# Optimization experiments

Measured on AMD Instinct MI355X. Metric: run time of the kernel, lower is better.

## Reference

```python
import jax, jax.numpy as jnp
import numpy as np

NCF = 256  # line_emb out features; must equal x channels C


def setup_inputs() -> dict:
    key = jax.random.key(0)
    k1, k2, k3 = jax.random.split(key, 3)
    x = jax.random.normal(k1, (16, 256, 128, 128), dtype=jnp.float32)
    attr = jax.random.normal(k2, (16, 64), dtype=jnp.float32)
    # nn.Linear(1, ncf, bias=False).weight has shape (ncf, 1); flatten to (ncf,)
    w_emb = jax.random.normal(k3, (NCF,), dtype=jnp.float32) / jnp.sqrt(jnp.float32(1.0))
    return {"x": x, "attr": attr, "w_emb": w_emb}


def reference(x, attr, w_emb):
    B, C, H, W = x.shape
    A = attr.reshape(B, -1).shape[1]
    # Linear(1, ncf): attr (B, A, 1) -> (B, A, ncf) is just an outer product
    sa_t = attr.reshape(B, A, 1) * w_emb[None, None, :]          # (B, A, ncf)
    xf = x.reshape(B, C, H * W)                                   # (B, C, HW)
    # tm = semantic_attr_t @ x : contract ncf (== C)
    tm = jnp.einsum('bac,bcn->ban', sa_t, xf)                     # (B, A, HW)
    p = jax.nn.softmax(tm, axis=0)                                # softmax over BATCH dim (dim=0)
    # fattn = semantic_attr (B, ncf, A) @ p (B, A, HW)
    fattn = jnp.einsum('bac,ban->bcn', sa_t, p)                   # (B, C, HW)
    return fattn.reshape(B, C, H, W)
```

## Files before the change

kernel.cpp:

```cpp
#include <hip/hip_runtime.h>
#include <math.h>

#define B_  16
#define C_  256
#define A_  64
#define HW_ 16384
#define HW4 (HW_ / 4)

__global__ __launch_bounds__(256) void k_y(const float* __restrict__ x,
                                           const float* __restrict__ w_emb,
                                           float4* __restrict__ y) {
    __shared__ float w[C_];
    for (int i = threadIdx.x; i < C_; i += 256) w[i] = w_emb[i];
    __syncthreads();

    const int idx = blockIdx.x * 256 + threadIdx.x;
    const int n4  = idx & (HW4 - 1);
    const int b   = idx >> 12;

    const float4* xp = (const float4*)(x + (size_t)b * C_ * HW_) + n4;
    float4 acc = {0.f, 0.f, 0.f, 0.f};
    #pragma unroll 8
    for (int c = 0; c < C_; ++c) {
        const float4 v = xp[(size_t)c * HW4];
        const float wc = w[c];
        acc.x += wc * v.x; acc.y += wc * v.y;
        acc.z += wc * v.z; acc.w += wc * v.w;
    }
    y[idx] = acc;
}

__global__ __launch_bounds__(64) void k_s(const float* __restrict__ y,
                                          const float* __restrict__ attr,
                                          float* __restrict__ s) {
    __shared__ float at[B_ * A_];
    for (int i = threadIdx.x; i < B_ * A_; i += 64) at[i] = attr[i];
    __syncthreads();

    const int n = blockIdx.x * 64 + threadIdx.x;

    float yv[B_];
    #pragma unroll
    for (int b = 0; b < B_; ++b) yv[b] = y[b * HW_ + n];

    float acc[B_];
    #pragma unroll
    for (int b = 0; b < B_; ++b) acc[b] = 0.f;

    for (int a = 0; a < A_; ++a) {
        float t[B_];
        float m = -INFINITY;
        #pragma unroll
        for (int b = 0; b < B_; ++b) {
            t[b] = at[b * A_ + a] * yv[b];
            m = fmaxf(m, t[b]);
        }
        float e[B_];
        float Z = 0.f;
        #pragma unroll
        for (int b = 0; b < B_; ++b) {
            e[b] = expf(t[b] - m);
            Z += e[b];
        }
        const float invZ = 1.f / Z;
        #pragma unroll
        for (int b = 0; b < B_; ++b)
            acc[b] += at[b * A_ + a] * e[b] * invZ;
    }

    #pragma unroll
    for (int b = 0; b < B_; ++b) s[b * HW_ + n] = acc[b];
}

__global__ __launch_bounds__(256) void k_out(const float4* __restrict__ s,
                                             const float* __restrict__ w_emb,
                                             float4* __restrict__ out) {
    __shared__ float w[C_];
    for (int i = threadIdx.x; i < C_; i += 256) w[i] = w_emb[i];
    __syncthreads();

    const int idx = blockIdx.x * 256 + threadIdx.x;
    const int n4  = idx & (HW4 - 1);
    const int b   = idx >> 12;

    const float4 sv = s[idx];
    const size_t base = (size_t)b * C_ * HW4 + n4;
    #pragma unroll 8
    for (int c = 0; c < C_; ++c) {
        const float wc = w[c];
        float4 o;
        o.x = wc * sv.x; o.y = wc * sv.y;
        o.z = wc * sv.z; o.w = wc * sv.w;
        out[base + (size_t)c * HW4] = o;
    }
}

extern "C" void kernel_launch(void* const* d_in, const int* in_sizes, int n_in,
                              void* d_out, int out_size, void* d_ws, size_t ws_size,
                              hipStream_t stream) {
    const float* x     = (const float*)d_in[0];
    const float* attr  = (const float*)d_in[1];
    const float* w_emb = (const float*)d_in[2];
    float* out = (float*)d_out;

    float* y = (float*)d_ws;
    float* s = y + (size_t)B_ * HW_;

    k_y  <<<(B_ * HW4) / 256, 256, 0, stream>>>(x, w_emb, (float4*)y);
    k_s  <<<HW_ / 64,          64, 0, stream>>>(y, attr, s);
    k_out<<<(B_ * HW4) / 256, 256, 0, stream>>>((const float4*)s, w_emb, (float4*)out);
}
```

Before: 523.9 us.

## Split channel reduction and output write across 4 channel quarters for more blocks

The channel contraction in k_y is split into four quarters, each written as a partial sum that k_s adds back together. k_out likewise splits its channel loop into quarters, so both bandwidth-bound kernels launch four times as many blocks to fill more compute units. k_s moves from 64 to 256 threads per block and uses the fast __expf intrinsic. The cost is an extra partial-sum buffer in workspace, extra reads in k_s, and slightly lower accuracy in the exponential.

```diff
diff --git a/kernel.cpp b/kernel.cpp
--- a/kernel.cpp
+++ b/kernel.cpp
@@ -6,42 +6,51 @@
 #define A_  64
 #define HW_ 16384
 #define HW4 (HW_ / 4)
+#define QSPLIT 4
+#define CQ  (C_ / QSPLIT)
 
 __global__ __launch_bounds__(256) void k_y(const float* __restrict__ x,
                                            const float* __restrict__ w_emb,
-                                           float4* __restrict__ y) {
-    __shared__ float w[C_];
-    for (int i = threadIdx.x; i < C_; i += 256) w[i] = w_emb[i];
+                                           float4* __restrict__ ypart) {
+    const int q    = blockIdx.x >> 8;
+    const int idxw = ((blockIdx.x & 255) << 8) + threadIdx.x;
+    const int n4   = idxw & (HW4 - 1);
+    const int b    = idxw >> 12;
+
+    __shared__ float w[CQ];
+    if (threadIdx.x < CQ) w[threadIdx.x] = w_emb[q * CQ + threadIdx.x];
     __syncthreads();
 
-    const int idx = blockIdx.x * 256 + threadIdx.x;
-    const int n4  = idx & (HW4 - 1);
-    const int b   = idx >> 12;
-
-    const float4* xp = (const float4*)(x + (size_t)b * C_ * HW_) + n4;
+    const float4* xp = (const float4*)(x + (size_t)b * C_ * HW_) + (size_t)(q * CQ) * HW4 + n4;
     float4 acc = {0.f, 0.f, 0.f, 0.f};
     #pragma unroll 8
-    for (int c = 0; c < C_; ++c) {
+    for (int c = 0; c < CQ; ++c) {
         const float4 v = xp[(size_t)c * HW4];
         const float wc = w[c];
         acc.x += wc * v.x; acc.y += wc * v.y;
         acc.z += wc * v.z; acc.w += wc * v.w;
     }
-    y[idx] = acc;
+    ypart[(size_t)q * (B_ * HW4) + idxw] = acc;
 }
 
-__global__ __launch_bounds__(64) void k_s(const float* __restrict__ y,
-                                          const float* __restrict__ attr,
-                                          float* __restrict__ s) {
+__global__ __launch_bounds__(256) void k_s(const float* __restrict__ ypart,
+                                           const float* __restrict__ attr,
+                                           float* __restrict__ s) {
     __shared__ float at[B_ * A_];
-    for (int i = threadIdx.x; i < B_ * A_; i += 64) at[i] = attr[i];
+    for (int i = threadIdx.x; i < B_ * A_; i += 256) at[i] = attr[i];
     __syncthreads();
 
-    const int n = blockIdx.x * 64 + threadIdx.x;
+    const int n = blockIdx.x * 256 + threadIdx.x;
 
     float yv[B_];
     #pragma unroll
-    for (int b = 0; b < B_; ++b) yv[b] = y[b * HW_ + n];
+    for (int b = 0; b < B_; ++b) {
+        float v = 0.f;
+        #pragma unroll
+        for (int qq = 0; qq < QSPLIT; ++qq)
+            v += ypart[(size_t)qq * (B_ * HW_) + b * HW_ + n];
+        yv[b] = v;
+    }
 
     float acc[B_];
     #pragma unroll
@@ -55,11 +64,11 @@
             t[b] = at[b * A_ + a] * yv[b];
             m = fmaxf(m, t[b]);
         }
+        float Z = 0.f;
         float e[B_];
-        float Z = 0.f;
         #pragma unroll
         for (int b = 0; b < B_; ++b) {
-            e[b] = expf(t[b] - m);
+            e[b] = __expf(t[b] - m);
             Z += e[b];
         }
         const float invZ = 1.f / Z;
@@ -75,23 +84,24 @@
 __global__ __launch_bounds__(256) void k_out(const float4* __restrict__ s,
                                              const float* __restrict__ w_emb,
                                              float4* __restrict__ out) {
-    __shared__ float w[C_];
-    for (int i = threadIdx.x; i < C_; i += 256) w[i] = w_emb[i];
+    const int q    = blockIdx.x >> 8;
+    const int idxw = ((blockIdx.x & 255) << 8) + threadIdx.x;
+    const int n4   = idxw & (HW4 - 1);
+    const int b    = idxw >> 12;
+
+    __shared__ float w[CQ];
+    if (threadIdx.x < CQ) w[threadIdx.x] = w_emb[q * CQ + threadIdx.x];
     __syncthreads();
 
-    const int idx = blockIdx.x * 256 + threadIdx.x;
-    const int n4  = idx & (HW4 - 1);
-    const int b   = idx >> 12;
-
-    const float4 sv = s[idx];
-    const size_t base = (size_t)b * C_ * HW4 + n4;
+    const float4 sv = s[idxw];
+    float4* op = out + (size_t)b * C_ * HW4 + (size_t)(q * CQ) * HW4 + n4;
     #pragma unroll 8
-    for (int c = 0; c < C_; ++c) {
+    for (int c = 0; c < CQ; ++c) {
         const float wc = w[c];
         float4 o;
         o.x = wc * sv.x; o.y = wc * sv.y;
         o.z = wc * sv.z; o.w = wc * sv.w;
-        out[base + (size_t)c * HW4] = o;
+        op[(size_t)c * HW4] = o;
     }
 }
 
@@ -103,10 +113,10 @@
     const float* w_emb = (const float*)d_in[2];
     float* out = (float*)d_out;
 
-    float* y = (float*)d_ws;
-    float* s = y + (size_t)B_ * HW_;
+    float* ypart = (float*)d_ws;
+    float* s     = ypart + (size_t)QSPLIT * B_ * HW_;
 
-    k_y  <<<(B_ * HW4) / 256, 256, 0, stream>>>(x, w_emb, (float4*)y);
-    k_s  <<<HW_ / 64,          64, 0, stream>>>(y, attr, s);
-    k_out<<<(B_ * HW4) / 256, 256, 0, stream>>>((const float4*)s, w_emb, (float4*)out);
+    k_y  <<<QSPLIT * 256, 256, 0, stream>>>(x, w_emb, (float4*)ypart);
+    k_s  <<<HW_ / 256,    256, 0, stream>>>(ypart, attr, s);
+    k_out<<<QSPLIT * 256, 256, 0, stream>>>((const float4*)s, w_emb, (float4*)out);
 }
```

Measured after the change: 520.8 us. Within noise of the previous version (-0.6%).

## Fuse projection, batch softmax and output expansion into one tiled kernel

Applied to the files above, without the earlier changes.

Replaces the three-kernel pipeline with a single kernel where each block handles 64 pixels across all batches: computes the channel projection, the batch-dim softmax accumulation split across waves, and writes the outer-product output. It removes workspace round-trips and extra launches, and uses nontemporal loads/stores plus fast exp. In exchange only 256 blocks run with scalar loads, so memory-level parallelism may be limited.

```diff
diff --git a/kernel.cpp b/kernel.cpp
--- a/kernel.cpp
+++ b/kernel.cpp
@@ -5,93 +5,91 @@
 #define C_  256
 #define A_  64
 #define HW_ 16384
-#define HW4 (HW_ / 4)
+#define P_  64
 
-__global__ __launch_bounds__(256) void k_y(const float* __restrict__ x,
-                                           const float* __restrict__ w_emb,
-                                           float4* __restrict__ y) {
+__global__ __launch_bounds__(256) void k_fused(const float* __restrict__ x,
+                                               const float* __restrict__ attr,
+                                               const float* __restrict__ w_emb,
+                                               float* __restrict__ out) {
     __shared__ float w[C_];
-    for (int i = threadIdx.x; i < C_; i += 256) w[i] = w_emb[i];
+    __shared__ float at[B_ * A_];
+    __shared__ float y[B_][P_];
+    __shared__ float part[4][B_][P_];
+    __shared__ float s[B_][P_];
+
+    const int t    = threadIdx.x;
+    const int lane = t & 63;
+    const int wv   = t >> 6;
+    const int n0   = blockIdx.x * P_;
+
+    if (t < C_) w[t] = w_emb[t];
+    for (int i = t; i < B_ * A_; i += 256) at[i] = attr[i];
     __syncthreads();
 
-    const int idx = blockIdx.x * 256 + threadIdx.x;
-    const int n4  = idx & (HW4 - 1);
-    const int b   = idx >> 12;
-
-    const float4* xp = (const float4*)(x + (size_t)b * C_ * HW_) + n4;
-    float4 acc = {0.f, 0.f, 0.f, 0.f};
-    #pragma unroll 8
-    for (int c = 0; c < C_; ++c) {
-        const float4 v = xp[(size_t)c * HW4];
-        const float wc = w[c];
-        acc.x += wc * v.x; acc.y += wc * v.y;
-        acc.z += wc * v.z; acc.w += wc * v.w;
+    {
+        const float* xp = x + (size_t)(wv * 4) * C_ * HW_ + n0 + lane;
+        float acc[4] = {0.f, 0.f, 0.f, 0.f};
+        #pragma unroll 4
+        for (int c = 0; c < C_; ++c) {
+            const float wc = w[c];
+            #pragma unroll
+            for (int bb = 0; bb < 4; ++bb)
+                acc[bb] += wc * __builtin_nontemporal_load(
+                    xp + (size_t)bb * C_ * HW_ + (size_t)c * HW_);
+        }
+        #pragma unroll
+        for (int bb = 0; bb < 4; ++bb) y[wv * 4 + bb][lane] = acc[bb];
     }
-    y[idx] = acc;
-}
-
-__global__ __launch_bounds__(64) void k_s(const float* __restrict__ y,
-                                          const float* __restrict__ attr,
-                                          float* __restrict__ s) {
-    __shared__ float at[B_ * A_];
-    for (int i = threadIdx.x; i < B_ * A_; i += 64) at[i] = attr[i];
     __syncthreads();
 
-    const int n = blockIdx.x * 64 + threadIdx.x;
+    {
+        float yv[B_];
+        #pragma unroll
+        for (int b = 0; b < B_; ++b) yv[b] = y[b][lane];
+        float pacc[B_];
+        #pragma unroll
+        for (int b = 0; b < B_; ++b) pacc[b] = 0.f;
 
-    float yv[B_];
-    #pragma unroll
-    for (int b = 0; b < B_; ++b) yv[b] = y[b * HW_ + n];
+        for (int aa = 0; aa < 16; ++aa) {
+            const int a = wv * 16 + aa;
+            float tb[B_];
+            float m = -INFINITY;
+            #pragma unroll
+            for (int b = 0; b < B_; ++b) {
+                tb[b] = at[b * A_ + a] * yv[b];
+                m = fmaxf(m, tb[b]);
+            }
+            float e[B_];
+            float Z = 0.f;
+            #pragma unroll
+            for (int b = 0; b < B_; ++b) {
+                e[b] = __expf(tb[b] - m);
+                Z += e[b];
+            }
+            const float iZ = 1.f / Z;
+            #pragma unroll
+            for (int b = 0; b < B_; ++b)
+                pacc[b] += at[b * A_ + a] * e[b] * iZ;
+        }
+        #pragma unroll
+        for (int b = 0; b < B_; ++b) part[wv][b][lane] = pacc[b];
+    }
+    __syncthreads();
 
-    float acc[B_];
-    #pragma unroll
-    for (int b = 0; b < B_; ++b) acc[b] = 0.f;
-
-    for (int a = 0; a < A_; ++a) {
-        float t[B_];
-        float m = -INFINITY;
-        #pragma unroll
-        for (int b = 0; b < B_; ++b) {
-            t[b] = at[b * A_ + a] * yv[b];
-            m = fmaxf(m, t[b]);
-        }
-        float e[B_];
-        float Z = 0.f;
-        #pragma unroll
-        for (int b = 0; b < B_; ++b) {
-            e[b] = expf(t[b] - m);
-            Z += e[b];
-        }
-        const float invZ = 1.f / Z;
-        #pragma unroll
-        for (int b = 0; b < B_; ++b)
-            acc[b] += at[b * A_ + a] * e[b] * invZ;
+    for (int i = t; i < B_ * P_; i += 256) {
+        const int b = i >> 6, px = i & 63;
+        s[b][px] = part[0][b][px] + part[1][b][px] + part[2][b][px] + part[3][b][px];
     }
+    __syncthreads();
 
     #pragma unroll
-    for (int b = 0; b < B_; ++b) s[b * HW_ + n] = acc[b];
-}
-
-__global__ __launch_bounds__(256) void k_out(const float4* __restrict__ s,
-                                             const float* __restrict__ w_emb,
-                                             float4* __restrict__ out) {
-    __shared__ float w[C_];
-    for (int i = threadIdx.x; i < C_; i += 256) w[i] = w_emb[i];
-    __syncthreads();
-
-    const int idx = blockIdx.x * 256 + threadIdx.x;
-    const int n4  = idx & (HW4 - 1);
-    const int b   = idx >> 12;
-
-    const float4 sv = s[idx];
-    const size_t base = (size_t)b * C_ * HW4 + n4;
-    #pragma unroll 8
-    for (int c = 0; c < C_; ++c) {
-        const float wc = w[c];
-        float4 o;
-        o.x = wc * sv.x; o.y = wc * sv.y;
-        o.z = wc * sv.z; o.w = wc * sv.w;
-        out[base + (size_t)c * HW4] = o;
+    for (int bb = 0; bb < 4; ++bb) {
+        const int b = wv * 4 + bb;
+        const float sv = s[b][lane];
+        float* op = out + (size_t)b * C_ * HW_ + n0 + lane;
+        #pragma unroll 8
+        for (int c = 0; c < C_; ++c)
+            __builtin_nontemporal_store(w[c] * sv, op + (size_t)c * HW_);
     }
 }
 
@@ -103,10 +101,5 @@
     const float* w_emb = (const float*)d_in[2];
     float* out = (float*)d_out;
 
-    float* y = (float*)d_ws;
-    float* s = y + (size_t)B_ * HW_;
-
-    k_y  <<<(B_ * HW4) / 256, 256, 0, stream>>>(x, w_emb, (float4*)y);
-    k_s  <<<HW_ / 64,          64, 0, stream>>>(y, attr, s);
-    k_out<<<(B_ * HW4) / 256, 256, 0, stream>>>((const float4*)s, w_emb, (float4*)out);
+    k_fused<<<HW_ / P_, 256, 0, stream>>>(x, attr, w_emb, out);
 }
```

Result: faster. 436.0 us (-16.8%).
